# Kernel optimization log

Hardware: AMD Instinct MI355X
Metric: run time of the kernel (lower is better)

The kernel has to match this reference:

```python
import jax, jax.numpy as jnp
import numpy as np


def setup_inputs() -> dict:
    key = jax.random.key(0)
    x = jax.random.normal(key, (64, 512, 16, 16), dtype=jnp.float32)
    return {"x": x}


def reference(x):
    # x: [B, dim, h, w] -> covariance pooling y: [B, dim, dim]
    B, dim, h, w = x.shape
    M = h * w
    xf = x.reshape(B, dim, M)
    # I_hat = (1/M) I - (1/M^2) 11^T  (centering matrix scaled by 1/M)
    inv_M = jnp.asarray(1.0 / M, dtype=x.dtype)
    I_hat = inv_M * jnp.eye(M, dtype=x.dtype) - (inv_M * inv_M) * jnp.ones((M, M), dtype=x.dtype)
    # y = x @ I_hat @ x^T, I_hat broadcast over batch
    xI = jnp.einsum('bdm,mn->bdn', xf, I_hat)   # [B, dim, M]
    y = jnp.einsum('bdn,ben->bde', xI, xf)      # [B, dim, dim]
    return y
```

## Files before the change

kernel.cpp:

```cpp
#include <hip/hip_runtime.h>
#include <stdint.h>


typedef __attribute__((ext_vector_type(8))) short bf16x8;
typedef __attribute__((ext_vector_type(4))) float f32x4;

static __device__ __forceinline__ unsigned short f2bf(float f) {
    union { float f; uint32_t u; } c; c.f = f;
    uint32_t u = c.u;
    return (unsigned short)((u + 0x7FFFu + ((u >> 16) & 1u)) >> 16);
}

static __device__ __forceinline__ void cvt_store(f32x4 v0, f32x4 v1, float* psum,
                                                 unsigned short* dst) {
    v0 *= 0.0625f; v1 *= 0.0625f;
    *psum += (v0.x + v0.y + v0.z + v0.w) + (v1.x + v1.y + v1.z + v1.w);
    bf16x8 o;
    o[0] = (short)f2bf(v0.x); o[1] = (short)f2bf(v0.y);
    o[2] = (short)f2bf(v0.z); o[3] = (short)f2bf(v0.w);
    o[4] = (short)f2bf(v1.x); o[5] = (short)f2bf(v1.y);
    o[6] = (short)f2bf(v1.z); o[7] = (short)f2bf(v1.w);
    *(bf16x8*)dst = o;
}

__global__ __launch_bounds__(256) void covpool_fused(const float* __restrict__ x,
                                                     float* __restrict__ y) {
    __shared__ __align__(16) unsigned short As[128 * 32];
    __shared__ __align__(16) unsigned short Bs[128 * 32];
    __shared__ __align__(16) float Ep[32 * 132];
    __shared__ float muA[128];
    __shared__ float muB[128];

    const int xcd = blockIdx.x & 7;
    const int j   = blockIdx.x >> 3;
    const int b   = xcd * 8 + j / 10;
    const int t10 = j % 10;
    const unsigned code = (unsigned)((0xFBA7653210ULL >> (4 * t10)) & 15ULL);
    const int tm = code >> 2, tn = code & 3;
    const bool diag = (tm == tn);

    const float* Ag = x + ((size_t)b * 512 + tm * 128) * 256;
    const float* Bg = x + ((size_t)b * 512 + tn * 128) * 256;

    const int tid  = threadIdx.x;
    const int lane = tid & 63;
    const int wave = tid >> 6;
    const int wm = (wave >> 1) * 64;
    const int wn = (wave & 1) * 64;

    f32x4 acc[4][4] = {};
    float pA[2] = {0.f, 0.f}, pB[2] = {0.f, 0.f};

    const int rl  = lane & 15;
    const int q   = lane >> 4;
    const int swl = (q ^ ((rl >> 1) & 3)) * 8;
    const int srow = tid >> 2, schunk = tid & 3;

    f32x4 a0[2], a1[2], b0[2], b1[2];
#pragma unroll
    for (int t = 0; t < 2; ++t) {
        const float* g = Ag + (size_t)(t * 64 + srow) * 256 + schunk * 8;
        a0[t] = *(const f32x4*)g; a1[t] = *(const f32x4*)(g + 4);
        if (!diag) {
            const float* h = Bg + (size_t)(t * 64 + srow) * 256 + schunk * 8;
            b0[t] = *(const f32x4*)h; b1[t] = *(const f32x4*)(h + 4);
        }
    }

    for (int kk = 0; kk < 256; kk += 32) {
        __syncthreads();
#pragma unroll
        for (int t = 0; t < 2; ++t) {
            const int row  = t * 64 + srow;
            const int slot = schunk ^ ((row >> 1) & 3);
            cvt_store(a0[t], a1[t], &pA[t], As + row * 32 + slot * 8);
            if (!diag) cvt_store(b0[t], b1[t], &pB[t], Bs + row * 32 + slot * 8);
        }
        __syncthreads();
        if (kk < 224) {
#pragma unroll
            for (int t = 0; t < 2; ++t) {
                const float* g = Ag + (size_t)(t * 64 + srow) * 256 + (kk + 32) + schunk * 8;
                a0[t] = *(const f32x4*)g; a1[t] = *(const f32x4*)(g + 4);
                if (!diag) {
                    const float* h = Bg + (size_t)(t * 64 + srow) * 256 + (kk + 32) + schunk * 8;
                    b0[t] = *(const f32x4*)h; b1[t] = *(const f32x4*)(h + 4);
                }
            }
        }
        const unsigned short* Bsrc = diag ? As : Bs;
        bf16x8 af[4], bfr[4];
#pragma unroll
        for (int i = 0; i < 4; ++i)
            af[i] = *(const bf16x8*)(As + (wm + i * 16 + rl) * 32 + swl);
#pragma unroll
        for (int jj = 0; jj < 4; ++jj)
            bfr[jj] = *(const bf16x8*)(Bsrc + (wn + jj * 16 + rl) * 32 + swl);
#pragma unroll
        for (int i = 0; i < 4; ++i)
#pragma unroll
            for (int jj = 0; jj < 4; ++jj)
                acc[i][jj] = __builtin_amdgcn_mfma_f32_16x16x32_bf16(
                    af[i], bfr[jj], acc[i][jj], 0, 0, 0);
    }

#pragma unroll
    for (int t = 0; t < 2; ++t) {
        float s = pA[t];
        s += __shfl_xor(s, 1, 64); s += __shfl_xor(s, 2, 64);
        if (schunk == 0) muA[t * 64 + srow] = s * 0.0625f;
        if (!diag) {
            float sb = pB[t];
            sb += __shfl_xor(sb, 1, 64); sb += __shfl_xor(sb, 2, 64);
            if (schunk == 0) muB[t * 64 + srow] = sb * 0.0625f;
        }
    }
    const float* muBp = diag ? muA : muB;
    float* yb = y + (size_t)b * 512 * 512;

#pragma unroll
    for (int c = 0; c < 4; ++c) {
        __syncthreads();
        if ((wave >> 1) == (c >> 1)) {
            const int ii0 = 2 * (c & 1);
#pragma unroll
            for (int ii = 0; ii < 2; ++ii) {
                const int i = ii0 + ii;
#pragma unroll
                for (int jj = 0; jj < 4; ++jj) {
                    const int col = wn + jj * 16 + rl;
                    const float mb = muBp[col];
#pragma unroll
                    for (int r = 0; r < 4; ++r) {
                        const int row = wm + i * 16 + q * 4 + r;
                        Ep[(ii * 16 + q * 4 + r) * 132 + col] = acc[i][jj][r] - muA[row] * mb;
                    }
                }
            }
        }
        __syncthreads();
#pragma unroll
        for (int v = 0; v < 4; ++v) {
            const int flat = v * 256 + tid;
            const int rloc = flat >> 5, c4 = flat & 31;
            f32x4 val = *(const f32x4*)(Ep + rloc * 132 + c4 * 4);
            *(f32x4*)(yb + (size_t)(tm * 128 + c * 32 + rloc) * 512 + tn * 128 + c4 * 4) = val;
        }
        if (!diag) {
#pragma unroll
            for (int v = 0; v < 4; ++v) {
                const int id = v * 256 + tid;
                const int cc = id >> 3, g = id & 7;
                f32x4 val;
#pragma unroll
                for (int e = 0; e < 4; ++e)
                    val[e] = Ep[(g * 4 + e) * 132 + cc];
                *(f32x4*)(yb + (size_t)(tn * 128 + cc) * 512 + tm * 128 + c * 32 + g * 4) = val;
            }
        }
    }
}

extern "C" void kernel_launch(void* const* d_in, const int* in_sizes, int n_in,
                              void* d_out, int out_size, void* d_ws, size_t ws_size,
                              hipStream_t stream) {
    const float* x = (const float*)d_in[0];
    float* yout = (float*)d_out;
    (void)d_ws; (void)ws_size;
    covpool_fused<<<640, 256, 0, stream>>>(x, yout);
}
```

Measured before the change: 104.0 us.

## Double threads per block to 512, halving per-wave tile and staging work

The block grows from 4 to 8 waves. Each wave now computes a 32x64 sub-tile instead of 64x64, and each thread stages one row chunk per K step instead of two. The epilogue is remapped so each wave pair writes one 32-row chunk. The aim is more waves in flight for latency hiding and less register pressure per thread, at the cost of more barrier participants and less MFMA work per LDS fragment load.

Result: slower. 112.0 us (+7.7%).

```diff
diff --git a/kernel.cpp b/kernel.cpp
--- a/kernel.cpp
+++ b/kernel.cpp
@@ -23,8 +23,8 @@
     *(bf16x8*)dst = o;
 }
 
-__global__ __launch_bounds__(256) void covpool_fused(const float* __restrict__ x,
-                                                     float* __restrict__ y) {
+__global__ __launch_bounds__(512, 4) void covpool_fused(const float* __restrict__ x,
+                                                        float* __restrict__ y) {
     __shared__ __align__(16) unsigned short As[128 * 32];
     __shared__ __align__(16) unsigned short Bs[128 * 32];
     __shared__ __align__(16) float Ep[32 * 132];
@@ -45,74 +45,63 @@
     const int tid  = threadIdx.x;
     const int lane = tid & 63;
     const int wave = tid >> 6;
-    const int wm = (wave >> 1) * 64;
+    const int wm = (wave >> 1) * 32;
     const int wn = (wave & 1) * 64;
 
-    f32x4 acc[4][4] = {};
-    float pA[2] = {0.f, 0.f}, pB[2] = {0.f, 0.f};
+    f32x4 acc[2][4] = {};
+    float pA = 0.f, pB = 0.f;
 
     const int rl  = lane & 15;
     const int q   = lane >> 4;
     const int swl = (q ^ ((rl >> 1) & 3)) * 8;
     const int srow = tid >> 2, schunk = tid & 3;
+    const int slot = schunk ^ ((srow >> 1) & 3);
+    unsigned short* Adst = As + srow * 32 + slot * 8;
+    unsigned short* Bdst = Bs + srow * 32 + slot * 8;
+    const float* Asrc = Ag + (size_t)srow * 256 + schunk * 8;
+    const float* Bsrc = Bg + (size_t)srow * 256 + schunk * 8;
 
-    f32x4 a0[2], a1[2], b0[2], b1[2];
-#pragma unroll
-    for (int t = 0; t < 2; ++t) {
-        const float* g = Ag + (size_t)(t * 64 + srow) * 256 + schunk * 8;
-        a0[t] = *(const f32x4*)g; a1[t] = *(const f32x4*)(g + 4);
-        if (!diag) {
-            const float* h = Bg + (size_t)(t * 64 + srow) * 256 + schunk * 8;
-            b0[t] = *(const f32x4*)h; b1[t] = *(const f32x4*)(h + 4);
-        }
-    }
+    f32x4 a0, a1, b0, b1;
+    a0 = *(const f32x4*)Asrc; a1 = *(const f32x4*)(Asrc + 4);
+    if (!diag) { b0 = *(const f32x4*)Bsrc; b1 = *(const f32x4*)(Bsrc + 4); }
 
     for (int kk = 0; kk < 256; kk += 32) {
         __syncthreads();
-#pragma unroll
-        for (int t = 0; t < 2; ++t) {
-            const int row  = t * 64 + srow;
-            const int slot = schunk ^ ((row >> 1) & 3);
-            cvt_store(a0[t], a1[t], &pA[t], As + row * 32 + slot * 8);
-            if (!diag) cvt_store(b0[t], b1[t], &pB[t], Bs + row * 32 + slot * 8);
-        }
+        cvt_store(a0, a1, &pA, Adst);
+        if (!diag) cvt_store(b0, b1, &pB, Bdst);
         __syncthreads();
         if (kk < 224) {
-#pragma unroll
-            for (int t = 0; t < 2; ++t) {
-                const float* g = Ag + (size_t)(t * 64 + srow) * 256 + (kk + 32) + schunk * 8;
-                a0[t] = *(const f32x4*)g; a1[t] = *(const f32x4*)(g + 4);
-                if (!diag) {
-                    const float* h = Bg + (size_t)(t * 64 + srow) * 256 + (kk + 32) + schunk * 8;
-                    b0[t] = *(const f32x4*)h; b1[t] = *(const f32x4*)(h + 4);
-                }
+            a0 = *(const f32x4*)(Asrc + kk + 32);
+            a1 = *(const f32x4*)(Asrc + kk + 36);
+            if (!diag) {
+                b0 = *(const f32x4*)(Bsrc + kk + 32);
+                b1 = *(const f32x4*)(Bsrc + kk + 36);
             }
         }
-        const unsigned short* Bsrc = diag ? As : Bs;
-        bf16x8 af[4], bfr[4];
+        const unsigned short* Bsr = diag ? As : Bs;
+        bf16x8 af[2], bfr[4];
 #pragma unroll
-        for (int i = 0; i < 4; ++i)
+        for (int i = 0; i < 2; ++i)
             af[i] = *(const bf16x8*)(As + (wm + i * 16 + rl) * 32 + swl);
 #pragma unroll
         for (int jj = 0; jj < 4; ++jj)
-            bfr[jj] = *(const bf16x8*)(Bsrc + (wn + jj * 16 + rl) * 32 + swl);
+            bfr[jj] = *(const bf16x8*)(Bsr + (wn + jj * 16 + rl) * 32 + swl);
 #pragma unroll
-        for (int i = 0; i < 4; ++i)
+        for (int i = 0; i < 2; ++i)
 #pragma unroll
             for (int jj = 0; jj < 4; ++jj)
                 acc[i][jj] = __builtin_amdgcn_mfma_f32_16x16x32_bf16(
                     af[i], bfr[jj], acc[i][jj], 0, 0, 0);
     }
 
-#pragma unroll
-    for (int t = 0; t < 2; ++t) {
-        float s = pA[t];
+    {
+        float s = pA;
         s += __shfl_xor(s, 1, 64); s += __shfl_xor(s, 2, 64);
-        if (schunk == 0) muA[t * 64 + srow] = s * 0.0625f;
+        if (schunk == 0) muA[srow] = s * 0.0625f;
         if (!diag) {
-            float sb = pB[t];
+            float sb = pB;
             sb += __shfl_xor(sb, 1, 64); sb += __shfl_xor(sb, 2, 64);
-            if (schunk == 0) muB[t * 64 + srow] = sb * 0.0625f;
+            if (schunk == 0) muB[srow] = sb * 0.0625f;
         }
     }
     const float* muBp = diag ? muA : muB;
@@ -121,11 +110,9 @@
 #pragma unroll
     for (int c = 0; c < 4; ++c) {
         __syncthreads();
-        if ((wave >> 1) == (c >> 1)) {
-            const int ii0 = 2 * (c & 1);
+        if ((wave >> 1) == c) {
 #pragma unroll
-            for (int ii = 0; ii < 2; ++ii) {
-                const int i = ii0 + ii;
+            for (int i = 0; i < 2; ++i) {
 #pragma unroll
                 for (int jj = 0; jj < 4; ++jj) {
                     const int col = wn + jj * 16 + rl;
@@ -133,23 +120,23 @@
 #pragma unroll
                     for (int r = 0; r < 4; ++r) {
                         const int row = wm + i * 16 + q * 4 + r;
-                        Ep[(ii * 16 + q * 4 + r) * 132 + col] = acc[i][jj][r] - muA[row] * mb;
+                        Ep[(i * 16 + q * 4 + r) * 132 + col] = acc[i][jj][r] - muA[row] * mb;
                     }
                 }
             }
         }
         __syncthreads();
 #pragma unroll
-        for (int v = 0; v < 4; ++v) {
-            const int flat = v * 256 + tid;
+        for (int v = 0; v < 2; ++v) {
+            const int flat = v * 512 + tid;
             const int rloc = flat >> 5, c4 = flat & 31;
             f32x4 val = *(const f32x4*)(Ep + rloc * 132 + c4 * 4);
             *(f32x4*)(yb + (size_t)(tm * 128 + c * 32 + rloc) * 512 + tn * 128 + c4 * 4) = val;
         }
         if (!diag) {
 #pragma unroll
-            for (int v = 0; v < 4; ++v) {
-                const int id = v * 256 + tid;
+            for (int v = 0; v < 2; ++v) {
+                const int id = v * 512 + tid;
                 const int cc = id >> 3, g = id & 7;
                 f32x4 val;
 #pragma unroll
@@ -167,5 +154,5 @@
     const float* x = (const float*)d_in[0];
     float* yout = (float*)d_out;
     (void)d_ws; (void)ws_size;
-    covpool_fused<<<640, 256, 0, stream>>>(x, yout);
+    covpool_fused<<<640, 512, 0, stream>>>(x, yout);
 }
```

## Double-buffer LDS tiles, single barrier per k-step, full-tile epilogue with nontemporal stores

Applied to the files above, without the earlier changes.

Reworks the main loop to double-buffer the bf16 A/B tiles in LDS. The next tile is converted and stored after the MFMAs, with one barrier per iteration instead of two. The epilogue writes the whole 128x128 result tile into a reused shared buffer in one pass instead of four 32-row chunks, and emits both the tile and its transpose with nontemporal stores. The 1/16 prescale before bf16 conversion moves to a 1/256 scale on the accumulators, and launch bounds request two blocks per CU. The larger shared footprint (~68KB) and the removed prescale may change occupancy and bf16 rounding behaviour.

Measured after the change: 107.6 us. 3.4% more time.

```diff
diff --git a/kernel.cpp b/kernel.cpp
--- a/kernel.cpp
+++ b/kernel.cpp
@@ -13,7 +13,6 @@
 
 static __device__ __forceinline__ void cvt_store(f32x4 v0, f32x4 v1, float* psum,
                                                  unsigned short* dst) {
-    v0 *= 0.0625f; v1 *= 0.0625f;
     *psum += (v0.x + v0.y + v0.z + v0.w) + (v1.x + v1.y + v1.z + v1.w);
     bf16x8 o;
     o[0] = (short)f2bf(v0.x); o[1] = (short)f2bf(v0.y);
@@ -23,13 +22,18 @@
     *(bf16x8*)dst = o;
 }
 
-__global__ __launch_bounds__(256) void covpool_fused(const float* __restrict__ x,
-                                                     float* __restrict__ y) {
-    __shared__ __align__(16) unsigned short As[128 * 32];
-    __shared__ __align__(16) unsigned short Bs[128 * 32];
-    __shared__ __align__(16) float Ep[32 * 132];
+static __device__ __forceinline__ void bar_lds() {
+    asm volatile("s_waitcnt lgkmcnt(0)" ::: "memory");
+    __builtin_amdgcn_s_barrier();
+    asm volatile("" ::: "memory");
+}
+
+__global__ __launch_bounds__(256, 2) void covpool_fused(const float* __restrict__ x,
+                                                        float* __restrict__ y) {
+    __shared__ __align__(16) float shf[128 * 132];
     __shared__ float muA[128];
     __shared__ float muB[128];
+    unsigned short* const Sbase = (unsigned short*)shf;
 
     const int xcd = blockIdx.x & 7;
     const int j   = blockIdx.x >> 3;
@@ -55,6 +59,7 @@
     const int q   = lane >> 4;
     const int swl = (q ^ ((rl >> 1) & 3)) * 8;
     const int srow = tid >> 2, schunk = tid & 3;
+    const int slot = schunk ^ ((srow >> 1) & 3);
 
     f32x4 a0[2], a1[2], b0[2], b1[2];
 #pragma unroll
@@ -66,97 +71,116 @@
             b0[t] = *(const f32x4*)h; b1[t] = *(const f32x4*)(h + 4);
         }
     }
+#pragma unroll
+    for (int t = 0; t < 2; ++t) {
+        const int row = t * 64 + srow;
+        cvt_store(a0[t], a1[t], &pA[t], Sbase + row * 32 + slot * 8);
+        if (!diag) cvt_store(b0[t], b1[t], &pB[t], Sbase + 8192 + row * 32 + slot * 8);
+    }
+#pragma unroll
+    for (int t = 0; t < 2; ++t) {
+        const float* g = Ag + (size_t)(t * 64 + srow) * 256 + 32 + schunk * 8;
+        a0[t] = *(const f32x4*)g; a1[t] = *(const f32x4*)(g + 4);
+        if (!diag) {
+            const float* h = Bg + (size_t)(t * 64 + srow) * 256 + 32 + schunk * 8;
+            b0[t] = *(const f32x4*)h; b1[t] = *(const f32x4*)(h + 4);
+        }
+    }
+    bar_lds();
 
-    for (int kk = 0; kk < 256; kk += 32) {
-        __syncthreads();
 #pragma unroll
-        for (int t = 0; t < 2; ++t) {
-            const int row  = t * 64 + srow;
-            const int slot = schunk ^ ((row >> 1) & 3);
-            cvt_store(a0[t], a1[t], &pA[t], As + row * 32 + slot * 8);
-            if (!diag) cvt_store(b0[t], b1[t], &pB[t], Bs + row * 32 + slot * 8);
-        }
-        __syncthreads();
-        if (kk < 224) {
-#pragma unroll
-            for (int t = 0; t < 2; ++t) {
-                const float* g = Ag + (size_t)(t * 64 + srow) * 256 + (kk + 32) + schunk * 8;
-                a0[t] = *(const f32x4*)g; a1[t] = *(const f32x4*)(g + 4);
-                if (!diag) {
-                    const float* h = Bg + (size_t)(t * 64 + srow) * 256 + (kk + 32) + schunk * 8;
-                    b0[t] = *(const f32x4*)h; b1[t] = *(const f32x4*)(h + 4);
-                }
-            }
-        }
-        const unsigned short* Bsrc = diag ? As : Bs;
+    for (int kk = 0; kk < 8; ++kk) {
+        const unsigned short* Acur = Sbase + (kk & 1) * 4096;
+        const unsigned short* Bcur = diag ? Acur : (Sbase + 8192 + (kk & 1) * 4096);
         bf16x8 af[4], bfr[4];
 #pragma unroll
         for (int i = 0; i < 4; ++i)
-            af[i] = *(const bf16x8*)(As + (wm + i * 16 + rl) * 32 + swl);
+            af[i] = *(const bf16x8*)(Acur + (wm + i * 16 + rl) * 32 + swl);
 #pragma unroll
         for (int jj = 0; jj < 4; ++jj)
-            bfr[jj] = *(const bf16x8*)(Bsrc + (wn + jj * 16 + rl) * 32 + swl);
+            bfr[jj] = *(const bf16x8*)(Bcur + (wn + jj * 16 + rl) * 32 + swl);
 #pragma unroll
         for (int i = 0; i < 4; ++i)
 #pragma unroll
             for (int jj = 0; jj < 4; ++jj)
                 acc[i][jj] = __builtin_amdgcn_mfma_f32_16x16x32_bf16(
                     af[i], bfr[jj], acc[i][jj], 0, 0, 0);
+        if (kk < 7) {
+            const int nb = (kk + 1) & 1;
+#pragma unroll
+            for (int t = 0; t < 2; ++t) {
+                const int row = t * 64 + srow;
+                cvt_store(a0[t], a1[t], &pA[t], Sbase + nb * 4096 + row * 32 + slot * 8);
+                if (!diag) cvt_store(b0[t], b1[t], &pB[t],
+                                     Sbase + 8192 + nb * 4096 + row * 32 + slot * 8);
+            }
+            if (kk < 6) {
+#pragma unroll
+                for (int t = 0; t < 2; ++t) {
+                    const float* g = Ag + (size_t)(t * 64 + srow) * 256 + (kk + 2) * 32 + schunk * 8;
+                    a0[t] = *(const f32x4*)g; a1[t] = *(const f32x4*)(g + 4);
+                    if (!diag) {
+                        const float* h = Bg + (size_t)(t * 64 + srow) * 256 + (kk + 2) * 32 + schunk * 8;
+                        b0[t] = *(const f32x4*)h; b1[t] = *(const f32x4*)(h + 4);
+                    }
+                }
+            }
+            bar_lds();
+        }
     }
 
 #pragma unroll
     for (int t = 0; t < 2; ++t) {
         float s = pA[t];
         s += __shfl_xor(s, 1, 64); s += __shfl_xor(s, 2, 64);
-        if (schunk == 0) muA[t * 64 + srow] = s * 0.0625f;
+        if (schunk == 0) muA[t * 64 + srow] = s * (1.0f / 256.0f);
         if (!diag) {
             float sb = pB[t];
             sb += __shfl_xor(sb, 1, 64); sb += __shfl_xor(sb, 2, 64);
-            if (schunk == 0) muB[t * 64 + srow] = sb * 0.0625f;
+            if (schunk == 0) muB[t * 64 + srow] = sb * (1.0f / 256.0f);
         }
     }
+    bar_lds();
+
     const float* muBp = diag ? muA : muB;
     float* yb = y + (size_t)b * 512 * 512;
+    const float inv256 = 1.0f / 256.0f;
 
 #pragma unroll
-    for (int c = 0; c < 4; ++c) {
-        __syncthreads();
-        if ((wave >> 1) == (c >> 1)) {
-            const int ii0 = 2 * (c & 1);
+    for (int i = 0; i < 4; ++i)
 #pragma unroll
-            for (int ii = 0; ii < 2; ++ii) {
-                const int i = ii0 + ii;
+        for (int jj = 0; jj < 4; ++jj) {
+            const int col = wn + jj * 16 + rl;
+            const float mb = muBp[col];
 #pragma unroll
-                for (int jj = 0; jj < 4; ++jj) {
-                    const int col = wn + jj * 16 + rl;
-                    const float mb = muBp[col];
-#pragma unroll
-                    for (int r = 0; r < 4; ++r) {
-                        const int row = wm + i * 16 + q * 4 + r;
-                        Ep[(ii * 16 + q * 4 + r) * 132 + col] = acc[i][jj][r] - muA[row] * mb;
-                    }
-                }
+            for (int r = 0; r < 4; ++r) {
+                const int row = wm + i * 16 + q * 4 + r;
+                shf[row * 132 + col] = acc[i][jj][r] * inv256 - muA[row] * mb;
             }
         }
-        __syncthreads();
+    bar_lds();
+
 #pragma unroll
-        for (int v = 0; v < 4; ++v) {
-            const int flat = v * 256 + tid;
-            const int rloc = flat >> 5, c4 = flat & 31;
-            f32x4 val = *(const f32x4*)(Ep + rloc * 132 + c4 * 4);
-            *(f32x4*)(yb + (size_t)(tm * 128 + c * 32 + rloc) * 512 + tn * 128 + c4 * 4) = val;
-        }
-        if (!diag) {
+    for (int v = 0; v < 16; ++v) {
+        const int flat = v * 256 + tid;
+        const int rloc = flat >> 5, c4 = flat & 31;
+        f32x4 val = *(const f32x4*)(shf + rloc * 132 + c4 * 4);
+        __builtin_nontemporal_store(
+            val, (f32x4*)(yb + (size_t)(tm * 128 + rloc) * 512 + tn * 128 + c4 * 4));
+    }
+    if (!diag) {
 #pragma unroll
-            for (int v = 0; v < 4; ++v) {
-                const int id = v * 256 + tid;
-                const int cc = id >> 3, g = id & 7;
-                f32x4 val;
+        for (int v = 0; v < 16; ++v) {
+            const int id   = v * 256 + tid;
+            const int cseg = id >> 10;
+            const int cc   = (id >> 3) & 127;
+            const int g    = id & 7;
+            f32x4 val;
 #pragma unroll
-                for (int e = 0; e < 4; ++e)
-                    val[e] = Ep[(g * 4 + e) * 132 + cc];
-                *(f32x4*)(yb + (size_t)(tn * 128 + cc) * 512 + tm * 128 + c * 32 + g * 4) = val;
-            }
+            for (int e = 0; e < 4; ++e)
+                val[e] = shf[(cseg * 32 + g * 4 + e) * 132 + cc];
+            __builtin_nontemporal_store(
+                val, (f32x4*)(yb + (size_t)(tn * 128 + cc) * 512 + tm * 128 + cseg * 32 + g * 4));
         }
     }
 }
```
